# Kernel optimization log

Measured on AMD Instinct MI355X. Metric: run time of the kernel, lower is better.

## Reference

```python
import jax, jax.numpy as jnp
import numpy as np

N = 50000     # nodes
E = 800000    # edges
D = 64        # hidesize (= out_channels per head)
H = 5         # heads
C = 64        # per-head channels (concat=False -> mean over heads, C == D)
NEG_SLOPE = 0.2
LN_EPS = 1e-5


def setup_inputs() -> dict:
    key = jax.random.key(0)
    ks = jax.random.split(key, 16)
    s = 0.05
    return {
        "features": jax.random.normal(ks[0], (N, D), dtype=jnp.float32),
        "edge_index": jax.random.randint(ks[1], (2, E), 0, N, dtype=jnp.int64),
        "rel_emb_vector": jax.random.normal(ks[2], (E, D), dtype=jnp.float32),
        # GATv2Conv params
        "Wl": jax.random.normal(ks[3], (D, H * C), dtype=jnp.float32) * s,
        "bl": jnp.zeros((H * C,), jnp.float32),
        "Wr": jax.random.normal(ks[4], (D, H * C), dtype=jnp.float32) * s,
        "br": jnp.zeros((H * C,), jnp.float32),
        "We": jax.random.normal(ks[5], (D, H * C), dtype=jnp.float32) * s,  # lin_edge, no bias
        "att": jax.random.normal(ks[6], (H, C), dtype=jnp.float32) * s,
        "conv_bias": jnp.zeros((C,), jnp.float32),
        # LayerNorms
        "ln_g": jnp.ones((D,), jnp.float32), "ln_b": jnp.zeros((D,), jnp.float32),
        "ln1_g": jnp.ones((D,), jnp.float32), "ln1_b": jnp.zeros((D,), jnp.float32),
        # MLP (activation resolved to None by the source bug)
        "fc_w": jax.random.normal(ks[7], (D, 2 * D), dtype=jnp.float32) * s,
        "fc_b": jnp.zeros((2 * D,), jnp.float32),
        "fc1_w": jax.random.normal(ks[8], (2 * D, D), dtype=jnp.float32) * s,
        "fc1_b": jnp.zeros((D,), jnp.float32),
    }


def _layernorm(x, g, b):
    m = x.mean(-1, keepdims=True)
    v = ((x - m) ** 2).mean(-1, keepdims=True)
    return (x - m) * jax.lax.rsqrt(v + LN_EPS) * g + b


def _gatv2_conv(x, edge_index, edge_attr, Wl, bl, Wr, br, We, att, conv_bias):
    src, dst = edge_index[0], edge_index[1]
    n = x.shape[0]
    # add_self_loops with fill_value='mean': self-loop edge_attr = mean of incoming edge_attr
    cnt = jax.ops.segment_sum(jnp.ones((edge_attr.shape[0],), x.dtype), dst, num_segments=n)
    loop_attr = jax.ops.segment_sum(edge_attr, dst, num_segments=n) / jnp.maximum(cnt, 1.0)[:, None]
    ar = jnp.arange(n, dtype=src.dtype)
    src2 = jnp.concatenate([src, ar])
    dst2 = jnp.concatenate([dst, ar])
    ea = jnp.concatenate([edge_attr, loop_attr], axis=0)        # [E+N, D]
    xl = (x @ Wl + bl).reshape(n, H, C)                          # source transform
    xr = (x @ Wr + br).reshape(n, H, C)                          # target transform
    em = (ea @ We).reshape(-1, H, C)
    m = jax.nn.leaky_relu(xl[src2] + xr[dst2] + em, NEG_SLOPE)   # [E+N, H, C]
    logits = jnp.einsum('ehc,hc->eh', m, att)                    # [E+N, H]
    # scatter-softmax over destination nodes (self loops guarantee nonempty segments)
    mx = jax.lax.stop_gradient(jax.ops.segment_max(logits, dst2, num_segments=n))
    z = jnp.exp(logits - mx[dst2])
    den = jax.ops.segment_sum(z, dst2, num_segments=n)
    alpha = z / den[dst2]                                        # [E+N, H]
    out = jax.ops.segment_sum(xl[src2] * alpha[:, :, None], dst2, num_segments=n)  # [N, H, C]
    return out.mean(axis=1) + conv_bias                          # concat=False -> head mean


def reference(features, edge_index, rel_emb_vector, Wl, bl, Wr, br, We, att, conv_bias,
              ln_g, ln_b, ln1_g, ln1_b, fc_w, fc_b, fc1_w, fc1_b):
    conv = _gatv2_conv(features, edge_index, rel_emb_vector, Wl, bl, Wr, br, We, att, conv_bias)
    x = _layernorm(features + conv, ln_g, ln_b)
    h = (x @ fc_w + fc_b) @ fc1_w + fc1_b   # activation=None, dropout in eval mode
    return _layernorm(x + h, ln1_g, ln1_b)
```

## Files before the change

### kernel.cpp

```cpp
#include <hip/hip_runtime.h>
#include <hip/hip_bf16.h>
#include <math.h>

#define LN_EPS 1e-5f
#define NEGS 0.2f

typedef short s8v __attribute__((ext_vector_type(8)));
typedef short s4v __attribute__((ext_vector_type(4)));
typedef float f4v __attribute__((ext_vector_type(4)));
typedef unsigned short ushort;

__device__ __forceinline__ float wredsum(float v) {
#pragma unroll
    for (int s = 32; s > 0; s >>= 1) v += __shfl_xor(v, s);
    return v;
}
__device__ __forceinline__ ushort f2bf(float x) {
    unsigned int u = __float_as_uint(x);
    u += 0x7fffu + ((u >> 16) & 1u);
    return (ushort)(u >> 16);
}
__device__ __forceinline__ float bf2f(ushort u) {
    return __uint_as_float(((unsigned int)u) << 16);
}

__global__ __launch_bounds__(256) void k_prep(const float* __restrict__ Weg,
                                              const float* __restrict__ Wlg,
                                              const float* __restrict__ Wrg,
                                              ushort* __restrict__ weTg,
                                              ushort* __restrict__ wlrTg) {
    int i = blockIdx.x * 256 + threadIdx.x;
    if (i >= 7680) return;
    int mat = i / 2560;
    int j = i - mat * 2560;
    int n = j >> 3, kb = j & 7;
    const float* W = (mat == 0) ? Weg : (mat == 1) ? Wlg : Wrg;
    s8v v;
#pragma unroll
    for (int k = 0; k < 8; k++) v[k] = (short)f2bf(W[(kb * 8 + k) * 320 + n]);
    int by = (n * 128 + kb * 16) ^ ((n & 7) << 4);
    ushort* dstp = (mat == 0) ? weTg : (wlrTg + (mat - 1) * 20480);
    *(s8v*)((char*)dstp + by) = v;
}

__global__ void k_hist(const int* __restrict__ dst, int* __restrict__ cnt, int E) {
    int idx = blockIdx.x * blockDim.x + threadIdx.x;
    int stride = gridDim.x * blockDim.x;
    for (; idx < E; idx += stride) atomicAdd(&cnt[dst[idx]], 1);
}

__global__ __launch_bounds__(1024) void k_scanA(const int* __restrict__ cnt,
                                                int* __restrict__ bsum, int N) {
    __shared__ int ws[16];
    int tt = threadIdx.x, ln = tt & 63, wv = tt >> 6;
    int i = blockIdx.x * 1024 + tt;
    int v = (i < N) ? (cnt[i] + 1) : 0;
#pragma unroll
    for (int s = 32; s > 0; s >>= 1) v += __shfl_xor(v, s);
    if (ln == 0) ws[wv] = v;
    __syncthreads();
    if (tt == 0) {
        int s = 0;
#pragma unroll
        for (int k = 0; k < 16; k++) s += ws[k];
        bsum[blockIdx.x] = s;
    }
}
__global__ __launch_bounds__(64) void k_scanB(const int* __restrict__ bsum,
                                              int* __restrict__ bpre,
                                              int* __restrict__ roffN, int nb) {
    int ln = threadIdx.x;
    int v = (ln < nb) ? bsum[ln] : 0;
    int x = v;
#pragma unroll
    for (int off = 1; off < 64; off <<= 1) {
        int y = __shfl_up(x, off);
        if (ln >= off) x += y;
    }
    if (ln < nb) bpre[ln] = x - v;
    if (ln == 63) *roffN = x;
}
__global__ __launch_bounds__(1024) void k_scanC(const int* __restrict__ cnt,
                                                const int* __restrict__ bpre,
                                                int* __restrict__ roff,
                                                int* __restrict__ wpos, int N) {
    __shared__ int ws[16];
    int tt = threadIdx.x, ln = tt & 63, wv = tt >> 6;
    int i = blockIdx.x * 1024 + tt;
    int v = (i < N) ? (cnt[i] + 1) : 0;
    int x = v;
#pragma unroll
    for (int off = 1; off < 64; off <<= 1) {
        int y = __shfl_up(x, off);
        if (ln >= off) x += y;
    }
    if (ln == 63) ws[wv] = x;
    __syncthreads();
    if (wv == 0) {
        int wsv = (ln < 16) ? ws[ln] : 0;
        int xs = wsv;
#pragma unroll
        for (int off = 1; off < 16; off <<= 1) {
            int y = __shfl_up(xs, off);
            if (ln >= off) xs += y;
        }
        if (ln < 16) ws[ln] = xs - wsv;
    }
    __syncthreads();
    int excl = x - v + ws[wv] + bpre[blockIdx.x];
    if (i < N) { roff[i] = excl; wpos[i] = excl; }
}

__global__ void k_scatter(const int* __restrict__ src, const int* __restrict__ dst,
                          int* __restrict__ wpos, int* __restrict__ eidC,
                          int* __restrict__ srcC, int* __restrict__ dstC, int E) {
    int idx = blockIdx.x * blockDim.x + threadIdx.x;
    int stride = gridDim.x * blockDim.x;
    for (; idx < E; idx += stride) {
        int d = dst[idx];
        int p = atomicAdd(&wpos[d], 1);
        eidC[p] = idx;
        srcC[p] = src[idx];
        dstC[p] = d;
    }
}

__global__ __launch_bounds__(256) void k_loopcsr(const int* __restrict__ eidC_ro,
                                                 const int* __restrict__ roff,
                                                 const float* __restrict__ rel,
                                                 float* __restrict__ loopat,
                                                 ushort* __restrict__ relbf,
                                                 int* __restrict__ eidC,
                                                 int* __restrict__ srcC,
                                                 int* __restrict__ dstC, int N, int E) {
    int t = threadIdx.x, ln = t & 63, wv = t >> 6;
    int nw = gridDim.x * 4;
    for (int n = blockIdx.x * 4 + wv; n < N; n += nw) {
        int r0 = roff[n], r1 = roff[n + 1];
        int deg = r1 - r0 - 1;
        float s0 = 0.f, s1 = 0.f, s2 = 0.f, s3 = 0.f;
        if (relbf) {
            int j = 0;
            for (; j + 4 <= deg; j += 4) {
                int e0 = eidC_ro[r0 + j], e1 = eidC_ro[r0 + j + 1];
                int e2 = eidC_ro[r0 + j + 2], e3 = eidC_ro[r0 + j + 3];
                float v0 = rel[(long long)e0 * 64 + ln];
                float v1 = rel[(long long)e1 * 64 + ln];
                float v2 = rel[(long long)e2 * 64 + ln];
                float v3 = rel[(long long)e3 * 64 + ln];
                s0 += v0; s1 += v1; s2 += v2; s3 += v3;
                relbf[(long long)(r0 + j) * 64 + ln] = f2bf(v0);
                relbf[(long long)(r0 + j + 1) * 64 + ln] = f2bf(v1);
                relbf[(long long)(r0 + j + 2) * 64 + ln] = f2bf(v2);
                relbf[(long long)(r0 + j + 3) * 64 + ln] = f2bf(v3);
            }
            for (; j < deg; j++) {
                float v = rel[(long long)eidC_ro[r0 + j] * 64 + ln];
                s0 += v;
                relbf[(long long)(r0 + j) * 64 + ln] = f2bf(v);
            }
            float s = (s0 + s1) + (s2 + s3);
            float mean = s / (float)(deg > 0 ? deg : 1);
            relbf[(long long)(r1 - 1) * 64 + ln] = f2bf(mean);
        } else {
            int j = 0;
            for (; j + 4 <= deg; j += 4) {
                int e0 = eidC_ro[r0 + j], e1 = eidC_ro[r0 + j + 1];
                int e2 = eidC_ro[r0 + j + 2], e3 = eidC_ro[r0 + j + 3];
                s0 += rel[(long long)e0 * 64 + ln];
                s1 += rel[(long long)e1 * 64 + ln];
                s2 += rel[(long long)e2 * 64 + ln];
                s3 += rel[(long long)e3 * 64 + ln];
            }
            for (; j < deg; j++) s0 += rel[(long long)eidC_ro[r0 + j] * 64 + ln];
            float s = (s0 + s1) + (s2 + s3);
            loopat[(long long)n * 64 + ln] = s / (float)(deg > 0 ? deg : 1);
        }
        if (ln == 0) {
            eidC[r1 - 1] = E + n;
            srcC[r1 - 1] = n;
            dstC[r1 - 1] = n;
        }
    }
}

__global__ __launch_bounds__(512) void k_linC(const float* __restrict__ feat,
                                              const ushort* __restrict__ wlrTg,
                                              const float* __restrict__ blg,
                                              const float* __restrict__ brg,
                                              ushort* __restrict__ xlbf,
                                              ushort* __restrict__ xrbf, int N) {
    __shared__ __align__(16) ushort wT[2][64 * 320];
    int t = threadIdx.x;
    {
        const s8v* wsrc = (const s8v*)wlrTg;
        s8v* wdst = (s8v*)&wT[0][0];
        for (int i = t; i < 5120; i += 512) wdst[i] = wsrc[i];
    }
    __syncthreads();

    int l = t & 63, wv = t >> 6;
    int g = l >> 4, m = l & 15;
    int wstride = gridDim.x * 128;
    for (int r0 = (blockIdx.x * 8 + wv) * 16; r0 < N; r0 += wstride) {
        s8v afr[2];
        {
            long long row = (r0 + m < N) ? (r0 + m) : (N - 1);
#pragma unroll
            for (int kh = 0; kh < 2; kh++) {
                const float* p = feat + row * 64 + kh * 32 + g * 8;
                float4 u0 = *(const float4*)(p);
                float4 u1 = *(const float4*)(p + 4);
                s8v a;
                a[0] = (short)f2bf(u0.x); a[1] = (short)f2bf(u0.y);
                a[2] = (short)f2bf(u0.z); a[3] = (short)f2bf(u0.w);
                a[4] = (short)f2bf(u1.x); a[5] = (short)f2bf(u1.y);
                a[6] = (short)f2bf(u1.z); a[7] = (short)f2bf(u1.w);
                afr[kh] = a;
            }
        }
#pragma unroll
        for (int mat = 0; mat < 2; mat++) {
            const float* bias = mat ? brg : blg;
            ushort* y = mat ? xrbf : xlbf;
            const char* wb = (const char*)&wT[mat][0];
#pragma unroll
            for (int h = 0; h < 5; h++) {
                f4v acc[4];
#pragma unroll
                for (int ct = 0; ct < 4; ct++) acc[ct] = (f4v)0.0f;
#pragma unroll
                for (int ct = 0; ct < 4; ct++) {
                    int n = h * 64 + ct * 16 + m;
                    int b0 = (n * 128 + 0 * 64 + g * 16) ^ ((n & 7) << 4);
                    int b1 = (n * 128 + 1 * 64 + g * 16) ^ ((n & 7) << 4);
                    s8v bf0 = *(const s8v*)(wb + b0);
                    s8v bf1 = *(const s8v*)(wb + b1);
                    acc[ct] = __builtin_amdgcn_mfma_f32_16x16x32_bf16(afr[0], bf0, acc[ct], 0, 0, 0);
                    acc[ct] = __builtin_amdgcn_mfma_f32_16x16x32_bf16(afr[1], bf1, acc[ct], 0, 0, 0);
                }
                float bv[4];
#pragma unroll
                for (int ct = 0; ct < 4; ct++) bv[ct] = bias[h * 64 + ct * 16 + m];
#pragma unroll
                for (int q = 0; q < 4; q++) {
                    int row = r0 + g * 4 + q;
                    if (row < N) {
                        s4v o;
#pragma unroll
                        for (int ct = 0; ct < 4; ct++) o[ct] = (short)f2bf(acc[ct][q] + bv[ct]);
                        *(s4v*)(y + (long long)row * 320 + h * 64 + m * 4) = o;
                    }
                }
            }
        }
    }
}

template <bool RELBF>
__global__ __launch_bounds__(512) void k_fused(
    const float* __restrict__ rel, const float* __restrict__ loopat,
    const ushort* __restrict__ relbf,
    const int* __restrict__ eidC, const int* __restrict__ srcC,
    const int* __restrict__ dstC,
    const ushort* __restrict__ xlbf, const ushort* __restrict__ xrbf,
    const ushort* __restrict__ weTg, const float* __restrict__ attg,
    float* __restrict__ zC, int E, int M) {
    __shared__ __align__(16) ushort weT[64 * 320];
    int t = threadIdx.x;
    {
        const s8v* wsrc = (const s8v*)weTg;
        s8v* wdst = (s8v*)weT;
        for (int i = t; i < 2560; i += 512) wdst[i] = wsrc[i];
    }
    __syncthreads();

    int l = t & 63, wv = t >> 6;
    int g = l >> 4, m = l & 15;
    int r0 = (blockIdx.x * 8 + wv) * 16;
    if (r0 >= M) return;

    s8v afr[2];
    if constexpr (RELBF) {
        int slot = r0 + m;
        if (slot >= M) slot = M - 1;
        const ushort* p = relbf + (long long)slot * 64 + g * 8;
        afr[0] = *(const s8v*)(p);
        afr[1] = *(const s8v*)(p + 32);
    } else {
        int slot = r0 + m;
        if (slot >= M) slot = M - 1;
        int e = eidC[slot];
        const float* ap = (e < E) ? (rel + (long long)e * 64)
                                  : (loopat + (long long)(e - E) * 64);
#pragma unroll
        for (int kh = 0; kh < 2; kh++) {
            const float* p = ap + kh * 32 + g * 8;
            float4 u0 = *(const float4*)(p);
            float4 u1 = *(const float4*)(p + 4);
            s8v a;
            a[0] = (short)f2bf(u0.x); a[1] = (short)f2bf(u0.y);
            a[2] = (short)f2bf(u0.z); a[3] = (short)f2bf(u0.w);
            a[4] = (short)f2bf(u1.x); a[5] = (short)f2bf(u1.y);
            a[6] = (short)f2bf(u1.z); a[7] = (short)f2bf(u1.w);
            afr[kh] = a;
        }
    }

    const ushort* xptr[4];
    const ushort* rptr[4];
    bool vld[4];
    int sarr[4];
#pragma unroll
    for (int q = 0; q < 4; q++) {
        int slot = r0 + g * 4 + q;
        vld[q] = slot < M;
        int ss = vld[q] ? slot : (M - 1);
        sarr[q] = ss;
        int s = srcC[ss], d = dstC[ss];
        xptr[q] = xlbf + (long long)s * 320 + m * 4;
        rptr[q] = xrbf + (long long)d * 320 + m * 4;
    }

    s4v xb[2][4], rb[2][4];
    float attb[2][4];
#pragma unroll
    for (int q = 0; q < 4; q++) {
        xb[0][q] = *(const s4v*)(xptr[q]);
        rb[0][q] = *(const s4v*)(rptr[q]);
    }
#pragma unroll
    for (int ct = 0; ct < 4; ct++) attb[0][ct] = attg[ct * 16 + m];

#pragma unroll
    for (int h = 0; h < 5; h++) {
        if (h < 4) {
#pragma unroll
            for (int q = 0; q < 4; q++) {
                xb[(h + 1) & 1][q] = *(const s4v*)(xptr[q] + (h + 1) * 64);
                rb[(h + 1) & 1][q] = *(const s4v*)(rptr[q] + (h + 1) * 64);
            }
#pragma unroll
            for (int ct = 0; ct < 4; ct++)
                attb[(h + 1) & 1][ct] = attg[(h + 1) * 64 + ct * 16 + m];
        }

        f4v acc[4];
#pragma unroll
        for (int ct = 0; ct < 4; ct++) acc[ct] = (f4v)0.0f;
        __builtin_amdgcn_s_setprio(1);
#pragma unroll
        for (int ct = 0; ct < 4; ct++) {
            int n = h * 64 + ct * 16 + m;
            int b0 = (n * 128 + 0 * 64 + g * 16) ^ ((n & 7) << 4);
            int b1 = (n * 128 + 1 * 64 + g * 16) ^ ((n & 7) << 4);
            s8v bf0 = *(const s8v*)((const char*)weT + b0);
            s8v bf1 = *(const s8v*)((const char*)weT + b1);
            acc[ct] = __builtin_amdgcn_mfma_f32_16x16x32_bf16(afr[0], bf0, acc[ct], 0, 0, 0);
            acc[ct] = __builtin_amdgcn_mfma_f32_16x16x32_bf16(afr[1], bf1, acc[ct], 0, 0, 0);
        }
        __builtin_amdgcn_s_setprio(0);

#pragma unroll
        for (int q = 0; q < 4; q++) {
            float sum = 0.f;
#pragma unroll
            for (int ct = 0; ct < 4; ct++) {
                float v = acc[ct][q] + bf2f((ushort)xb[h & 1][q][ct])
                                     + bf2f((ushort)rb[h & 1][q][ct]);
                v = v > 0.f ? v : v * NEGS;
                sum = fmaf(v, attb[h & 1][ct], sum);
            }
            sum += __shfl_xor(sum, 1);
            sum += __shfl_xor(sum, 2);
            sum += __shfl_xor(sum, 4);
            sum += __shfl_xor(sum, 8);
            if (vld[q] && m == 0)
                zC[(long long)sarr[q] * 5 + h] = __expf(sum);
        }
    }
}

__global__ __launch_bounds__(256) void k_agg(const float* __restrict__ zC,
                                             const int* __restrict__ srcC,
                                             const int* __restrict__ roff,
                                             const ushort* __restrict__ xlbf,
                                             float* __restrict__ conv, int N) {
    int t = threadIdx.x, ln = t & 63, wv = t >> 6;
    int sub = ln >> 4, m = ln & 15;
    int nw = gridDim.x * 4;
    for (int n = blockIdx.x * 4 + wv; n < N; n += nw) {
        int r0 = roff[n], r1 = roff[n + 1];
        int deg = r1 - r0;
        float se[5] = {0.f, 0.f, 0.f, 0.f, 0.f};
        float accv[5][4];
#pragma unroll
        for (int h = 0; h < 5; h++)
#pragma unroll
            for (int j = 0; j < 4; j++) accv[h][j] = 0.f;
        for (int jj = sub; jj < deg; jj += 4) {
            int slot = r0 + jj;
            int s = srcC[slot];
            const ushort* xp = xlbf + (long long)s * 320 + m * 4;
            long long lb = (long long)slot * 5;
#pragma unroll
            for (int h = 0; h < 5; h++) {
                float z = zC[lb + h];
                se[h] += z;
                s4v xv = *(const s4v*)(xp + h * 64);
#pragma unroll
                for (int j = 0; j < 4; j++)
                    accv[h][j] = fmaf(z, bf2f((ushort)xv[j]), accv[h][j]);
            }
        }
        float dh[5];
#pragma unroll
        for (int h = 0; h < 5; h++) dh[h] = 16.0f / wredsum(se[h]);
        float tot[4];
#pragma unroll
        for (int j = 0; j < 4; j++) {
            float v = 0.f;
#pragma unroll
            for (int h = 0; h < 5; h++) v = fmaf(accv[h][j], dh[h], v);
            v += __shfl_xor(v, 16);
            v += __shfl_xor(v, 32);
            tot[j] = v;
        }
        float v0 = __shfl(tot[0], m);
        float v1 = __shfl(tot[1], m);
        float v2 = __shfl(tot[2], m);
        float v3 = __shfl(tot[3], m);
        float outv = (sub == 0) ? v0 : (sub == 1) ? v1 : (sub == 2) ? v2 : v3;
        conv[(long long)n * 64 + ln] = outv * 0.2f;
    }
}

__global__ __launch_bounds__(512) void k_mlp(const float* __restrict__ feat,
                                             const float* __restrict__ conv,
                                             const float* __restrict__ cbias,
                                             const float* __restrict__ lng,
                                             const float* __restrict__ lnb,
                                             const float* __restrict__ ln1g,
                                             const float* __restrict__ ln1b,
                                             const float* __restrict__ fcwg,
                                             const float* __restrict__ fcb,
                                             const float* __restrict__ fc1wg,
                                             const float* __restrict__ fc1b,
                                             float* __restrict__ out, int N) {
    __shared__ __align__(16) ushort w1T[64 * 128];
    __shared__ __align__(16) ushort w2T[64 * 128];
    __shared__ __align__(16) ushort tls[8][16 * 128];
    __shared__ __align__(16) ushort xnl[8][16 * 64];
    int t = threadIdx.x;
    for (int i = t; i < 8192; i += 512) {
        int k = i >> 7, n = i & 127;
        int by = (n * 128 + k * 2) ^ ((n & 7) << 4);
        w1T[by >> 1] = f2bf(fcwg[i]);
    }
    for (int i = t; i < 8192; i += 512) {
        int k = i >> 6, n = i & 63;
        int by = (n * 256 + k * 2) ^ ((n & 7) << 4);
        w2T[by >> 1] = f2bf(fc1wg[i]);
    }
    __syncthreads();
    int ln = t & 63, wv = t >> 6;
    int g = ln >> 4, m = ln & 15;
    char* tb = (char*)&tls[wv][0];
    char* xb = (char*)&xnl[wv][0];
    float fcbv[8];
#pragma unroll
    for (int ct = 0; ct < 8; ct++) fcbv[ct] = fcb[ct * 16 + m];
    float fc1bv[4], g1v[4], b1v[4];
#pragma unroll
    for (int ct = 0; ct < 4; ct++) {
        fc1bv[ct] = fc1b[ct * 16 + m];
        g1v[ct] = ln1g[ct * 16 + m];
        b1v[ct] = ln1b[ct * 16 + m];
    }
    int nblk = gridDim.x * 8;
    for (int nb0 = (blockIdx.x * 8 + wv) * 16; nb0 < N; nb0 += nblk * 16) {
        int node = nb0 + m;
        long long nd = (node < N) ? node : (N - 1);
        float xv[2][8];
#pragma unroll
        for (int kh = 0; kh < 2; kh++) {
            int c0 = kh * 32 + g * 8;
            const float* fp = feat + nd * 64 + c0;
            const float* cp = conv + nd * 64 + c0;
            float4 f0 = *(const float4*)fp, f1 = *(const float4*)(fp + 4);
            float4 q0 = *(const float4*)cp, q1 = *(const float4*)(cp + 4);
            float4 cb0 = *(const float4*)(cbias + c0), cb1 = *(const float4*)(cbias + c0 + 4);
            xv[kh][0] = f0.x + q0.x + cb0.x; xv[kh][1] = f0.y + q0.y + cb0.y;
            xv[kh][2] = f0.z + q0.z + cb0.z; xv[kh][3] = f0.w + q0.w + cb0.w;
            xv[kh][4] = f1.x + q1.x + cb1.x; xv[kh][5] = f1.y + q1.y + cb1.y;
            xv[kh][6] = f1.z + q1.z + cb1.z; xv[kh][7] = f1.w + q1.w + cb1.w;
        }
        float sm = 0.f;
#pragma unroll
        for (int kh = 0; kh < 2; kh++)
#pragma unroll
            for (int j = 0; j < 8; j++) sm += xv[kh][j];
        sm += __shfl_xor(sm, 16); sm += __shfl_xor(sm, 32);
        float mu = sm * (1.0f / 64.0f);
        float vr = 0.f;
#pragma unroll
        for (int kh = 0; kh < 2; kh++)
#pragma unroll
            for (int j = 0; j < 8; j++) {
                float dv = xv[kh][j] - mu;
                vr += dv * dv;
            }
        vr += __shfl_xor(vr, 16); vr += __shfl_xor(vr, 32);
        float rs = rsqrtf(vr * (1.0f / 64.0f) + LN_EPS);
        s8v af[2];
#pragma unroll
        for (int kh = 0; kh < 2; kh++) {
            int c0 = kh * 32 + g * 8;
            float4 g0 = *(const float4*)(lng + c0), g1 = *(const float4*)(lng + c0 + 4);
            float4 e0 = *(const float4*)(lnb + c0), e1 = *(const float4*)(lnb + c0 + 4);
            float gg[8] = {g0.x, g0.y, g0.z, g0.w, g1.x, g1.y, g1.z, g1.w};
            float bb[8] = {e0.x, e0.y, e0.z, e0.w, e1.x, e1.y, e1.z, e1.w};
#pragma unroll
            for (int j = 0; j < 8; j++)
                af[kh][j] = (short)f2bf((xv[kh][j] - mu) * rs * gg[j] + bb[j]);
            int by = (m * 128 + (kh * 32 + g * 8) * 2) ^ ((m & 7) << 4);
            *(s8v*)(xb + by) = af[kh];
        }
        f4v a1[8];
#pragma unroll
        for (int ct = 0; ct < 8; ct++) a1[ct] = (f4v)0.0f;
#pragma unroll
        for (int ct = 0; ct < 8; ct++) {
            int n1 = ct * 16 + m;
#pragma unroll
            for (int kh = 0; kh < 2; kh++) {
                int by = (n1 * 128 + (kh * 32 + g * 8) * 2) ^ ((n1 & 7) << 4);
                s8v bf = *(const s8v*)((const char*)w1T + by);
                a1[ct] = __builtin_amdgcn_mfma_f32_16x16x32_bf16(af[kh], bf, a1[ct], 0, 0, 0);
            }
        }
#pragma unroll
        for (int ct = 0; ct < 8; ct++)
#pragma unroll
            for (int q = 0; q < 4; q++) {
                int r = g * 4 + q, c = ct * 16 + m;
                int by = (r * 256 + c * 2) ^ ((r & 7) << 4);
                *(ushort*)(tb + by) = f2bf(a1[ct][q] + fcbv[ct]);
            }
        f4v a2[4];
#pragma unroll
        for (int ct = 0; ct < 4; ct++) a2[ct] = (f4v)0.0f;
#pragma unroll
        for (int kh2 = 0; kh2 < 4; kh2++) {
            int by = (m * 256 + (kh2 * 32 + g * 8) * 2) ^ ((m & 7) << 4);
            s8v a2f = *(const s8v*)(tb + by);
#pragma unroll
            for (int ct = 0; ct < 4; ct++) {
                int n2 = ct * 16 + m;
                int by2 = (n2 * 256 + (kh2 * 32 + g * 8) * 2) ^ ((n2 & 7) << 4);
                s8v bf = *(const s8v*)((const char*)w2T + by2);
                a2[ct] = __builtin_amdgcn_mfma_f32_16x16x32_bf16(a2f, bf, a2[ct], 0, 0, 0);
            }
        }
#pragma unroll
        for (int q = 0; q < 4; q++) {
            int r = g * 4 + q;
            float yv[4];
#pragma unroll
            for (int ct = 0; ct < 4; ct++) {
                int by = (r * 128 + (ct * 16 + m) * 2) ^ ((r & 7) << 4);
                yv[ct] = bf2f(*(const ushort*)(xb + by)) + a2[ct][q] + fc1bv[ct];
            }
            float sm2 = (yv[0] + yv[1]) + (yv[2] + yv[3]);
            sm2 += __shfl_xor(sm2, 1); sm2 += __shfl_xor(sm2, 2);
            sm2 += __shfl_xor(sm2, 4); sm2 += __shfl_xor(sm2, 8);
            float mu2 = sm2 * (1.0f / 64.0f);
            float vr2 = 0.f;
#pragma unroll
            for (int ct = 0; ct < 4; ct++) {
                float dv = yv[ct] - mu2;
                vr2 += dv * dv;
            }
            vr2 += __shfl_xor(vr2, 1); vr2 += __shfl_xor(vr2, 2);
            vr2 += __shfl_xor(vr2, 4); vr2 += __shfl_xor(vr2, 8);
            float rs2 = rsqrtf(vr2 * (1.0f / 64.0f) + LN_EPS);
            int rn = nb0 + r;
            if (rn < N) {
#pragma unroll
                for (int ct = 0; ct < 4; ct++)
                    out[(long long)rn * 64 + ct * 16 + m] =
                        (yv[ct] - mu2) * rs2 * g1v[ct] + b1v[ct];
            }
        }
    }
}

extern "C" void kernel_launch(void* const* d_in, const int* in_sizes, int n_in,
                              void* d_out, int out_size, void* d_ws, size_t ws_size,
                              hipStream_t stream) {
    const float* feat = (const float*)d_in[0];
    const int* ei = (const int*)d_in[1];
    const float* rel = (const float*)d_in[2];
    const float* Wl = (const float*)d_in[3];
    const float* bl = (const float*)d_in[4];
    const float* Wr = (const float*)d_in[5];
    const float* br = (const float*)d_in[6];
    const float* We = (const float*)d_in[7];
    const float* att = (const float*)d_in[8];
    const float* cbias = (const float*)d_in[9];
    const float* lng = (const float*)d_in[10];
    const float* lnb = (const float*)d_in[11];
    const float* ln1g = (const float*)d_in[12];
    const float* ln1b = (const float*)d_in[13];
    const float* fcw = (const float*)d_in[14];
    const float* fcb = (const float*)d_in[15];
    const float* fc1w = (const float*)d_in[16];
    const float* fc1b = (const float*)d_in[17];
    float* out = (float*)d_out;

    int N = in_sizes[0] / 64;
    int E = in_sizes[1] / 2;
    int M = E + N;
    const int* src = ei;
    const int* dst = ei + E;
    int nb = (N + 1023) / 1024;

    char* wsb = (char*)d_ws;
    ushort* xlbf = (ushort*)wsb;            wsb += (size_t)N * 320 * 2;
    ushort* xrbf = (ushort*)wsb;            wsb += (size_t)N * 320 * 2;
    float* loopat = (float*)wsb;            wsb += (size_t)N * 64 * 4;
    float* conv = (float*)wsb;              wsb += (size_t)N * 64 * 4;
    ushort* weTg = (ushort*)wsb;            wsb += 40960;
    ushort* wlrTg = (ushort*)wsb;           wsb += 81920;
    float* zC = (float*)wsb;                wsb += (size_t)M * 5 * 4;
    int* cnt = (int*)wsb;                   wsb += (size_t)N * 4;
    int* roff = (int*)wsb;                  wsb += (size_t)(N + 1) * 4;
    int* wpos = (int*)wsb;                  wsb += (size_t)N * 4;
    int* eidC = (int*)wsb;                  wsb += (size_t)M * 4;
    int* srcC = (int*)wsb;                  wsb += (size_t)M * 4;
    int* dstC = (int*)wsb;                  wsb += (size_t)M * 4;
    int* bsum = (int*)wsb;                  wsb += 64 * 4;
    int* bpre = (int*)wsb;                  wsb += 64 * 4;

    size_t used = (size_t)(wsb - (char*)d_ws);
    size_t roff_relbf = (used + 15) & ~(size_t)15;
    bool use_relbf = (roff_relbf + (size_t)M * 128) <= ws_size;
    ushort* relbf = use_relbf ? (ushort*)((char*)d_ws + roff_relbf) : nullptr;

    hipMemsetAsync(cnt, 0, (size_t)N * 4, stream);

    k_prep<<<30, 256, 0, stream>>>(We, Wl, Wr, weTg, wlrTg);
    k_hist<<<1024, 256, 0, stream>>>(dst, cnt, E);
    k_scanA<<<nb, 1024, 0, stream>>>(cnt, bsum, N);
    k_scanB<<<1, 64, 0, stream>>>(bsum, bpre, &roff[N], nb);
    k_scanC<<<nb, 1024, 0, stream>>>(cnt, bpre, roff, wpos, N);
    k_scatter<<<1024, 256, 0, stream>>>(src, dst, wpos, eidC, srcC, dstC, E);
    k_loopcsr<<<2048, 256, 0, stream>>>(eidC, roff, rel, loopat, relbf, eidC, srcC, dstC, N, E);
    k_linC<<<(N + 127) / 128, 512, 0, stream>>>(feat, wlrTg, bl, br, xlbf, xrbf, N);
    if (use_relbf)
        k_fused<true><<<(M + 127) / 128, 512, 0, stream>>>(rel, loopat, relbf, eidC, srcC, dstC,
                                                           xlbf, xrbf, weTg, att, zC, E, M);
    else
        k_fused<false><<<(M + 127) / 128, 512, 0, stream>>>(rel, loopat, relbf, eidC, srcC, dstC,
                                                            xlbf, xrbf, weTg, att, zC, E, M);
    k_agg<<<3200, 256, 0, stream>>>(zC, srcC, roff, xlbf, conv, N);
    k_mlp<<<391, 512, 0, stream>>>(feat, conv, cbias, lng, lnb, ln1g, ln1b, fcw, fcb, fc1w, fc1b,
                                   out, N);
}
```

Baseline: 507.6 us.

## Convert edge attributes to bf16 during CSR scatter and compute self-loop mean separately

```diff
diff --git a/kernel.cpp b/kernel.cpp
--- a/kernel.cpp
+++ b/kernel.cpp
@@ -125,11 +125,68 @@
     }
 }
 
+__global__ __launch_bounds__(256) void k_scatter2(const int* __restrict__ src,
+                                                  const int* __restrict__ dst,
+                                                  int* __restrict__ wpos,
+                                                  int* __restrict__ srcC,
+                                                  int* __restrict__ dstC,
+                                                  const float* __restrict__ rel,
+                                                  ushort* __restrict__ relbf, int E) {
+    int t = threadIdx.x;
+    int ln = t & 63, wv = t >> 6;
+    int sub = ln >> 4, m = ln & 15;
+    long long base = ((long long)blockIdx.x * 4 + wv) * 4;
+    long long stride = (long long)gridDim.x * 16;
+    for (long long e0 = base; e0 < E; e0 += stride) {
+        long long e = e0 + sub;
+        bool ok = e < E;
+        long long ee = ok ? e : (long long)(E - 1);
+        float4 v = *(const float4*)(rel + ee * 64 + m * 4);
+        int p = 0;
+        if (m == 0 && ok) {
+            int d = dst[ee];
+            p = atomicAdd(&wpos[d], 1);
+            srcC[p] = src[ee];
+            dstC[p] = d;
+        }
+        p = __shfl(p, sub * 16);
+        if (ok) {
+            s4v o;
+            o[0] = (short)f2bf(v.x); o[1] = (short)f2bf(v.y);
+            o[2] = (short)f2bf(v.z); o[3] = (short)f2bf(v.w);
+            *(s4v*)(relbf + (long long)p * 64 + m * 4) = o;
+        }
+    }
+}
+
+__global__ __launch_bounds__(256) void k_mean(const int* __restrict__ roff,
+                                              ushort* __restrict__ relbf,
+                                              int* __restrict__ srcC,
+                                              int* __restrict__ dstC, int N) {
+    int t = threadIdx.x, ln = t & 63, wv = t >> 6;
+    int nw = gridDim.x * 4;
+    for (int n = blockIdx.x * 4 + wv; n < N; n += nw) {
+        int r0 = roff[n], r1 = roff[n + 1];
+        int deg = r1 - r0 - 1;
+        float s0 = 0.f, s1 = 0.f, s2 = 0.f, s3 = 0.f;
+        int j = 0;
+        for (; j + 4 <= deg; j += 4) {
+            s0 += bf2f(relbf[(long long)(r0 + j) * 64 + ln]);
+            s1 += bf2f(relbf[(long long)(r0 + j + 1) * 64 + ln]);
+            s2 += bf2f(relbf[(long long)(r0 + j + 2) * 64 + ln]);
+            s3 += bf2f(relbf[(long long)(r0 + j + 3) * 64 + ln]);
+        }
+        for (; j < deg; j++) s0 += bf2f(relbf[(long long)(r0 + j) * 64 + ln]);
+        float s = (s0 + s1) + (s2 + s3);
+        relbf[(long long)(r1 - 1) * 64 + ln] = f2bf(s / (float)(deg > 0 ? deg : 1));
+        if (ln == 0) { srcC[r1 - 1] = n; dstC[r1 - 1] = n; }
+    }
+}
+
 __global__ __launch_bounds__(256) void k_loopcsr(const int* __restrict__ eidC_ro,
                                                  const int* __restrict__ roff,
                                                  const float* __restrict__ rel,
                                                  float* __restrict__ loopat,
-                                                 ushort* __restrict__ relbf,
                                                  int* __restrict__ eidC,
                                                  int* __restrict__ srcC,
                                                  int* __restrict__ dstC, int N, int E) {
@@ -139,43 +196,18 @@
         int r0 = roff[n], r1 = roff[n + 1];
         int deg = r1 - r0 - 1;
         float s0 = 0.f, s1 = 0.f, s2 = 0.f, s3 = 0.f;
-        if (relbf) {
-            int j = 0;
-            for (; j + 4 <= deg; j += 4) {
-                int e0 = eidC_ro[r0 + j], e1 = eidC_ro[r0 + j + 1];
-                int e2 = eidC_ro[r0 + j + 2], e3 = eidC_ro[r0 + j + 3];
-                float v0 = rel[(long long)e0 * 64 + ln];
-                float v1 = rel[(long long)e1 * 64 + ln];
-                float v2 = rel[(long long)e2 * 64 + ln];
-                float v3 = rel[(long long)e3 * 64 + ln];
-                s0 += v0; s1 += v1; s2 += v2; s3 += v3;
-                relbf[(long long)(r0 + j) * 64 + ln] = f2bf(v0);
-                relbf[(long long)(r0 + j + 1) * 64 + ln] = f2bf(v1);
-                relbf[(long long)(r0 + j + 2) * 64 + ln] = f2bf(v2);
-                relbf[(long long)(r0 + j + 3) * 64 + ln] = f2bf(v3);
-            }
-            for (; j < deg; j++) {
-                float v = rel[(long long)eidC_ro[r0 + j] * 64 + ln];
-                s0 += v;
-                relbf[(long long)(r0 + j) * 64 + ln] = f2bf(v);
-            }
-            float s = (s0 + s1) + (s2 + s3);
-            float mean = s / (float)(deg > 0 ? deg : 1);
-            relbf[(long long)(r1 - 1) * 64 + ln] = f2bf(mean);
-        } else {
-            int j = 0;
-            for (; j + 4 <= deg; j += 4) {
-                int e0 = eidC_ro[r0 + j], e1 = eidC_ro[r0 + j + 1];
-                int e2 = eidC_ro[r0 + j + 2], e3 = eidC_ro[r0 + j + 3];
-                s0 += rel[(long long)e0 * 64 + ln];
-                s1 += rel[(long long)e1 * 64 + ln];
-                s2 += rel[(long long)e2 * 64 + ln];
-                s3 += rel[(long long)e3 * 64 + ln];
-            }
-            for (; j < deg; j++) s0 += rel[(long long)eidC_ro[r0 + j] * 64 + ln];
-            float s = (s0 + s1) + (s2 + s3);
-            loopat[(long long)n * 64 + ln] = s / (float)(deg > 0 ? deg : 1);
-        }
+        int j = 0;
+        for (; j + 4 <= deg; j += 4) {
+            int e0 = eidC_ro[r0 + j], e1 = eidC_ro[r0 + j + 1];
+            int e2 = eidC_ro[r0 + j + 2], e3 = eidC_ro[r0 + j + 3];
+            s0 += rel[(long long)e0 * 64 + ln];
+            s1 += rel[(long long)e1 * 64 + ln];
+            s2 += rel[(long long)e2 * 64 + ln];
+            s3 += rel[(long long)e3 * 64 + ln];
+        }
+        for (; j < deg; j++) s0 += rel[(long long)eidC_ro[r0 + j] * 64 + ln];
+        float s = (s0 + s1) + (s2 + s3);
+        loopat[(long long)n * 64 + ln] = s / (float)(deg > 0 ? deg : 1);
         if (ln == 0) {
             eidC[r1 - 1] = E + n;
             srcC[r1 - 1] = n;
@@ -654,8 +686,13 @@
     k_scanA<<<nb, 1024, 0, stream>>>(cnt, bsum, N);
     k_scanB<<<1, 64, 0, stream>>>(bsum, bpre, &roff[N], nb);
     k_scanC<<<nb, 1024, 0, stream>>>(cnt, bpre, roff, wpos, N);
-    k_scatter<<<1024, 256, 0, stream>>>(src, dst, wpos, eidC, srcC, dstC, E);
-    k_loopcsr<<<2048, 256, 0, stream>>>(eidC, roff, rel, loopat, relbf, eidC, srcC, dstC, N, E);
+    if (use_relbf) {
+        k_scatter2<<<4096, 256, 0, stream>>>(src, dst, wpos, srcC, dstC, rel, relbf, E);
+        k_mean<<<2048, 256, 0, stream>>>(roff, relbf, srcC, dstC, N);
+    } else {
+        k_scatter<<<1024, 256, 0, stream>>>(src, dst, wpos, eidC, srcC, dstC, E);
+        k_loopcsr<<<2048, 256, 0, stream>>>(eidC, roff, rel, loopat, eidC, srcC, dstC, N, E);
+    }
     k_linC<<<(N + 127) / 128, 512, 0, stream>>>(feat, wlrTg, bl, br, xlbf, xrbf, N);
     if (use_relbf)
         k_fused<true><<<(M + 127) / 128, 512, 0, stream>>>(rel, loopat, relbf, eidC, srcC, dstC,
```

New measurement: 498.3 us. No clear change (-1.8%).
